# Performance work log

Hardware: AMD Instinct MI355X
Metric: run time of the kernel (lower is better)

## Reference

```python
import jax, jax.numpy as jnp
import numpy as np

B, E, S = 8, 128, 4096


def setup_inputs() -> dict:
    key = jax.random.key(0)
    ks = jax.random.split(key, 7)
    sc = 1.0 / np.sqrt(E)
    return {
        "x": jax.random.normal(ks[0], (B, E, S), dtype=jnp.float32),
        "Wq": jax.random.normal(ks[1], (E, E), dtype=jnp.float32) * sc,
        "bq": jax.random.normal(ks[2], (E,), dtype=jnp.float32) * 0.01,
        "Wk": jax.random.normal(ks[3], (E, E), dtype=jnp.float32) * sc,
        "bk": jax.random.normal(ks[4], (E,), dtype=jnp.float32) * 0.01,
        "Wv": jax.random.normal(ks[5], (E, E), dtype=jnp.float32) * sc,
        "bv": jax.random.normal(ks[6], (E,), dtype=jnp.float32) * 0.01,
    }


def reference(x, Wq, bq, Wk, bk, Wv, bv):
    # x: [B, E, S]; Conv1d(k=1) == per-position linear over channels.
    # Project then move to [B, S, E] (matches .permute(0, 2, 1)).
    Q = jnp.einsum('bes,fe->bsf', x, Wq) + bq  # [B, S, E]
    K = jnp.einsum('bes,fe->bsf', x, Wk) + bk
    V = jnp.einsum('bes,fe->bsf', x, Wv) + bv
    scale = jnp.sqrt(jnp.asarray(float(x.shape[1]), dtype=jnp.float32))
    attn = jnp.einsum('bqe,bke->bqk', Q, K) / scale  # [B, S, S]
    attn = jax.nn.softmax(attn, axis=2)
    out = jnp.einsum('bqk,bke->bqe', attn, V)  # [B, S, E]
    return out.transpose(0, 2, 1)  # [B, E, S]
```

## Files before the change

### kernel.cpp

```cpp
#include <hip/hip_runtime.h>
#include <math.h>

#define NB 8
#define NE 128
#define NS 4096
#define CSCALE 0.12751743f

typedef short s8v __attribute__((ext_vector_type(8)));
typedef float f4v __attribute__((ext_vector_type(4)));
typedef float f16v __attribute__((ext_vector_type(16)));
typedef unsigned int u32;
typedef unsigned int u2v __attribute__((ext_vector_type(2)));
typedef __attribute__((address_space(1))) const u32* gp1_t;
typedef __attribute__((address_space(3))) u32* lp3_t;

__device__ __forceinline__ ushort f2bf(float f) {
  union { float f; unsigned u; } v; v.f = f;
  unsigned r = v.u + 0x7fffu + ((v.u >> 16) & 1u);
  return (ushort)(r >> 16);
}
__device__ __forceinline__ float bf2f(ushort h) {
  union { unsigned u; float f; } v; v.u = ((unsigned)h) << 16; return v.f;
}
__device__ __forceinline__ void gload_lds16(const void* g, void* l) {
  __builtin_amdgcn_global_load_lds((gp1_t)g, (lp3_t)l, 16, 0, 0);
}
__device__ __forceinline__ u32 cvtpk(float lo, float hi) {
  u32 r;
  asm("v_cvt_pk_bf16_f32 %0, %1, %2" : "=v"(r) : "v"(lo), "v"(hi));
  return r;
}
__device__ __forceinline__ void split8(const float* __restrict__ p, float scale,
                                       s8v& hi, s8v& lo) {
  union { s8v v; ushort u[8]; } H, L;
  #pragma unroll
  for (int i = 0; i < 8; ++i) {
    float v = p[i] * scale;
    ushort h = f2bf(v);
    H.u[i] = h;
    L.u[i] = f2bf(v - bf2f(h));
  }
  hi = H.v; lo = L.v;
}

__global__ __launch_bounds__(256, 2) void proj_gemm(
    const float* __restrict__ x,
    const float* __restrict__ Wq, const float* __restrict__ bq,
    const float* __restrict__ Wk, const float* __restrict__ bk,
    const float* __restrict__ Wv, const float* __restrict__ bv,
    ushort* __restrict__ Qn, ushort* __restrict__ Kn, ushort* __restrict__ Vt)
{
  const int tid = threadIdx.x;
  const int wv = tid >> 6, lane = tid & 63;
  const int g = lane >> 4, c = lane & 15;
  const int bid = blockIdx.x;
  const int b = bid & 7;
  const int s0 = (bid >> 3) * 64;
  const float* xb = x + (size_t)b * NE * NS;

  __shared__ __align__(16) ushort xh[64][136], xl[64][136];

  {
    const int ss = tid & 63, cq = tid >> 6;
    #pragma unroll
    for (int p = 0; p < 4; ++p) {
      const int ch = p * 4 + cq;
      union { s8v v; ushort u[8]; } H, L;
      #pragma unroll
      for (int i = 0; i < 8; ++i) {
        float v = xb[(size_t)(ch * 8 + i) * NS + s0 + ss];
        ushort hi = f2bf(v);
        H.u[i] = hi;
        L.u[i] = f2bf(v - bf2f(hi));
      }
      *(s8v*)&xh[ss][ch * 8] = H.v;
      *(s8v*)&xl[ss][ch * 8] = L.v;
    }
  }
  __syncthreads();

  f4v aq[2][4], ak[2][4], av[2][4];
  #pragma unroll
  for (int i = 0; i < 2; ++i)
    #pragma unroll
    for (int j = 0; j < 4; ++j) {
      aq[i][j] = (f4v){0.f,0.f,0.f,0.f};
      ak[i][j] = (f4v){0.f,0.f,0.f,0.f};
      av[i][j] = (f4v){0.f,0.f,0.f,0.f};
    }

  #pragma unroll
  for (int ks = 0; ks < 4; ++ks) {
    s8v xbh[4], xbl[4];
    #pragma unroll
    for (int st = 0; st < 4; ++st) {
      xbh[st] = *(const s8v*)&xh[st * 16 + c][ks * 32 + g * 8];
      xbl[st] = *(const s8v*)&xl[st * 16 + c][ks * 32 + g * 8];
    }
    #pragma unroll
    for (int ftl = 0; ftl < 2; ++ftl) {
      const int f0 = (wv * 2 + ftl) * 16;
      const size_t wo = (size_t)(f0 + c) * NE + ks * 32 + g * 8;
      s8v qh, ql, kh, kl, vh, vl;
      split8(Wq + wo, CSCALE, qh, ql);
      split8(Wk + wo, 1.0f,   kh, kl);
      split8(Wv + wo, 1.0f,   vh, vl);
      #pragma unroll
      for (int st = 0; st < 4; ++st) {
        aq[ftl][st] = __builtin_amdgcn_mfma_f32_16x16x32_bf16(xbh[st], qh, aq[ftl][st], 0, 0, 0);
        aq[ftl][st] = __builtin_amdgcn_mfma_f32_16x16x32_bf16(xbl[st], qh, aq[ftl][st], 0, 0, 0);
        aq[ftl][st] = __builtin_amdgcn_mfma_f32_16x16x32_bf16(xbh[st], ql, aq[ftl][st], 0, 0, 0);
        av[ftl][st] = __builtin_amdgcn_mfma_f32_16x16x32_bf16(vh, xbh[st], av[ftl][st], 0, 0, 0);
        av[ftl][st] = __builtin_amdgcn_mfma_f32_16x16x32_bf16(vh, xbl[st], av[ftl][st], 0, 0, 0);
        av[ftl][st] = __builtin_amdgcn_mfma_f32_16x16x32_bf16(vl, xbh[st], av[ftl][st], 0, 0, 0);
        ak[ftl][st] = __builtin_amdgcn_mfma_f32_16x16x32_bf16(xbh[st], kh, ak[ftl][st], 0, 0, 0);
        ak[ftl][st] = __builtin_amdgcn_mfma_f32_16x16x32_bf16(xbl[st], kh, ak[ftl][st], 0, 0, 0);
        ak[ftl][st] = __builtin_amdgcn_mfma_f32_16x16x32_bf16(xbh[st], kl, ak[ftl][st], 0, 0, 0);
      }
    }
  }

  ushort* Qnb = Qn + (size_t)b * NS * NE;
  ushort* Knb = Kn + (size_t)b * NS * NE;
  ushort* Vtb = Vt + (size_t)b * NE * NS;
  #pragma unroll
  for (int ftl = 0; ftl < 2; ++ftl) {
    const int f0 = (wv * 2 + ftl) * 16;
    #pragma unroll
    for (int r = 0; r < 4; ++r) {
      const int f = f0 + 4 * g + r;
      const float bvv = bv[f];
      #pragma unroll
      for (int st = 0; st < 4; ++st)
        Vtb[(size_t)f * NS + s0 + st * 16 + c] = f2bf(av[ftl][st][r] + bvv);
    }
    const float bqv = bq[f0 + c] * CSCALE;
    const float bkv = bk[f0 + c];
    #pragma unroll
    for (int st = 0; st < 4; ++st)
      #pragma unroll
      for (int r = 0; r < 4; ++r) {
        const size_t ro = (size_t)(s0 + st * 16 + 4 * g + r) * NE + f0 + c;
        Qnb[ro] = f2bf(aq[ftl][st][r] + bqv);
        Knb[ro] = f2bf(ak[ftl][st][r] + bkv);
      }
  }
}

__global__ __launch_bounds__(256, 1) void attn_kernel(
    const ushort* __restrict__ Qn, const ushort* __restrict__ Kn,
    const ushort* __restrict__ Vt, float* __restrict__ out)
{
  const int tid = threadIdx.x;
  const int wv = tid >> 6, lane = tid & 63;
  const int h = lane >> 5, q5 = lane & 31;
  const int slice = wv >> 1;
  const int ws = wv & 1;
  const int bid = blockIdx.x;
  const int b = bid & 7;
  const int qw = (bid >> 3) * 128 + ws * 64;

  const ushort* Qb = Qn + (size_t)b * NS * NE;
  const char*   Kb = (const char*)(Kn + (size_t)b * NS * NE);
  const char*   Vb = (const char*)(Vt + (size_t)b * NE * NS);

  __shared__ __align__(16) char ldsK[2][2][16384];
  __shared__ __align__(16) char ldsV[2][2][16384];
  __shared__ float lx[2][2][32];

  s8v qf[2][8];
  #pragma unroll
  for (int u = 0; u < 2; ++u)
    #pragma unroll
    for (int dc = 0; dc < 8; ++dc)
      qf[u][dc] = *(const s8v*)(Qb + (size_t)(qw + u * 32 + q5) * NE + dc * 16 + h * 8);

  auto stage = [&](int buf, int t) {
    const int kt = slice * 32 + t;
    const char* Ksrc = Kb + (size_t)kt * (64 * 256);
    #pragma unroll
    for (int p = 0; p < 8; ++p) {
      const int off = ws * 8192 + p * 1024;
      const int lo = off + lane * 16;
      const int row = lo >> 8;
      gload_lds16(Ksrc + (lo ^ ((row & 15) << 4)), &ldsK[slice][buf][off]);
    }
    #pragma unroll
    for (int p = 0; p < 8; ++p) {
      const int off = ws * 8192 + p * 1024;
      const int lo = off + lane * 16;
      const int row = lo >> 7;
      const int inner = (lo & 127) ^ ((row & 7) << 4);
      gload_lds16(Vb + (size_t)row * (NS * 2) + kt * 128 + inner, &ldsV[slice][buf][off]);
    }
  };

  auto makefrag = [&](const float* p, int r0) -> s8v {
    u32 A = cvtpk(p[r0 + 0], p[r0 + 1]);
    u32 B = cvtpk(p[r0 + 4], p[r0 + 5]);
    u32 C = cvtpk(p[r0 + 2], p[r0 + 3]);
    u32 D = cvtpk(p[r0 + 6], p[r0 + 7]);
    u2v rAB = __builtin_amdgcn_permlane32_swap(A, B, false, false);
    u2v rCD = __builtin_amdgcn_permlane32_swap(C, D, false, false);
    union { s8v v; u32 w[4]; } P;
    P.w[0] = rAB[0]; P.w[1] = rCD[0]; P.w[2] = rAB[1]; P.w[3] = rCD[1];
    return P.v;
  };

  f16v oA[4], oB[4];
  #pragma unroll
  for (int dt = 0; dt < 4; ++dt) {
    oA[dt] = (f16v){0,0,0,0,0,0,0,0,0,0,0,0,0,0,0,0};
    oB[dt] = (f16v){0,0,0,0,0,0,0,0,0,0,0,0,0,0,0,0};
  }
  float lA = 0.f, lB = 0.f;

  stage(0, 0);
  asm volatile("s_waitcnt vmcnt(0)" ::: "memory");
  __syncthreads();

  #pragma unroll 1
  for (int t = 0; t < 32; ++t) {
    const int cur = t & 1;
    if (t + 1 < 32) stage(cur ^ 1, t + 1);
    const char* bK = ldsK[slice][cur];
    const char* bV = ldsV[slice][cur];

    #pragma unroll
    for (int kc = 0; kc < 2; ++kc) {
      f16v sA = (f16v){0,0,0,0,0,0,0,0,0,0,0,0,0,0,0,0};
      f16v sB = (f16v){0,0,0,0,0,0,0,0,0,0,0,0,0,0,0,0};
      #pragma unroll
      for (int dc = 0; dc < 8; ++dc) {
        s8v kf = *(const s8v*)(bK + (kc * 32 + q5) * 256 + ((dc * 32 + h * 16) ^ ((q5 & 15) << 4)));
        sA = __builtin_amdgcn_mfma_f32_32x32x16_bf16(kf, qf[0][dc], sA, 0, 0, 0);
        sB = __builtin_amdgcn_mfma_f32_32x32x16_bf16(kf, qf[1][dc], sB, 0, 0, 0);
      }
      float pA[16], pB[16];
      #pragma unroll
      for (int r = 0; r < 16; ++r) {
        pA[r] = __builtin_amdgcn_exp2f(sA[r]); lA += pA[r];
        pB[r] = __builtin_amdgcn_exp2f(sB[r]); lB += pB[r];
      }
      #pragma unroll
      for (int ksl = 0; ksl < 2; ++ksl) {
        s8v PA = makefrag(pA, ksl * 8);
        s8v PB = makefrag(pB, ksl * 8);
        const int ks = kc * 2 + ksl;
        #pragma unroll
        for (int dt = 0; dt < 4; ++dt) {
          s8v vf = *(const s8v*)(bV + (dt * 32 + q5) * 128 + ((ks * 32 + h * 16) ^ ((q5 & 7) << 4)));
          oA[dt] = __builtin_amdgcn_mfma_f32_32x32x16_bf16(vf, PA, oA[dt], 0, 0, 0);
          oB[dt] = __builtin_amdgcn_mfma_f32_32x32x16_bf16(vf, PB, oB[dt], 0, 0, 0);
        }
      }
    }
    asm volatile("s_waitcnt vmcnt(0)" ::: "memory");
    __syncthreads();
  }

  lA += __shfl_xor(lA, 32);
  lB += __shfl_xor(lB, 32);
  float* cb = (float*)&ldsK[0][0][0];
  if (slice == 1) {
    #pragma unroll
    for (int dt = 0; dt < 4; ++dt)
      #pragma unroll
      for (int r = 0; r < 16; ++r) {
        cb[ws * 8192 + (dt * 16 + r) * 64 + lane]      = oA[dt][r];
        cb[ws * 8192 + (64 + dt * 16 + r) * 64 + lane] = oB[dt][r];
      }
    if (h == 0) { lx[ws][0][q5] = lA; lx[ws][1][q5] = lB; }
  }
  __syncthreads();
  if (slice == 0) {
    const float rA = 1.0f / (lA + lx[ws][0][q5]);
    const float rB = 1.0f / (lB + lx[ws][1][q5]);
    float* ob = out + (size_t)b * NE * NS;
    #pragma unroll
    for (int dt = 0; dt < 4; ++dt)
      #pragma unroll
      for (int r = 0; r < 16; ++r) {
        const int e = dt * 32 + (r & 3) + 8 * (r >> 2) + 4 * h;
        ob[(size_t)e * NS + qw + q5] =
            (oA[dt][r] + cb[ws * 8192 + (dt * 16 + r) * 64 + lane]) * rA;
        ob[(size_t)e * NS + qw + 32 + q5] =
            (oB[dt][r] + cb[ws * 8192 + (64 + dt * 16 + r) * 64 + lane]) * rB;
      }
  }
}

extern "C" void kernel_launch(void* const* d_in, const int* in_sizes, int n_in,
                              void* d_out, int out_size, void* d_ws, size_t ws_size,
                              hipStream_t stream) {
  (void)in_sizes; (void)n_in; (void)out_size; (void)ws_size;
  const float* x  = (const float*)d_in[0];
  const float* Wq = (const float*)d_in[1];
  const float* bq = (const float*)d_in[2];
  const float* Wk = (const float*)d_in[3];
  const float* bk = (const float*)d_in[4];
  const float* Wv = (const float*)d_in[5];
  const float* bv = (const float*)d_in[6];
  float* out = (float*)d_out;

  ushort* Qn = (ushort*)d_ws;
  ushort* Kn = Qn + (size_t)NB * NS * NE;
  ushort* Vt = Kn + (size_t)NB * NS * NE;

  proj_gemm<<<dim3(NS / 64 * NB), 256, 0, stream>>>(x, Wq, bq, Wk, bk, Wv, bv, Qn, Kn, Vt);
  attn_kernel<<<dim3(NS / 128 * NB), 256, 0, stream>>>(Qn, Kn, Vt, out);
}
```

Baseline: 119.0 us.

## Split attention key range across four wave slices with 512-thread blocks

Each block now runs 8 waves instead of 4, so the key sequence is split into four slices of 32-key tiles instead of two slices of 64-key tiles. K and V staging is divided by wave group: one group loads K and the other loads V. The partial outputs and row sums from the four slices are combined through LDS in a serialized accumulation with a barrier per slice. The aim is more waves per CU to hide latency. The cost is a longer reduction epilogue and a tighter register budget from launch_bounds(512,2), which may cause spills given the large MFMA accumulators.

Result: slower. 131.5 us (+10.5%).

```diff
diff --git a/kernel.cpp b/kernel.cpp
--- a/kernel.cpp
+++ b/kernel.cpp
@@ -147,15 +147,15 @@
   }
 }
 
-__global__ __launch_bounds__(256, 1) void attn_kernel(
+__global__ __launch_bounds__(512, 2) void attn_kernel(
     const ushort* __restrict__ Qn, const ushort* __restrict__ Kn,
     const ushort* __restrict__ Vt, float* __restrict__ out)
 {
   const int tid = threadIdx.x;
   const int wv = tid >> 6, lane = tid & 63;
   const int h = lane >> 5, q5 = lane & 31;
-  const int slice = wv >> 1;
-  const int ws = wv & 1;
+  const int slice = wv & 3;
+  const int ws = wv >> 2;
   const int bid = blockIdx.x;
   const int b = bid & 7;
   const int qw = (bid >> 3) * 128 + ws * 64;
@@ -164,9 +164,11 @@
   const char*   Kb = (const char*)(Kn + (size_t)b * NS * NE);
   const char*   Vb = (const char*)(Vt + (size_t)b * NE * NS);
 
-  __shared__ __align__(16) char ldsK[2][2][16384];
-  __shared__ __align__(16) char ldsV[2][2][16384];
-  __shared__ float lx[2][2][32];
+  __shared__ __align__(16) char lds[131072];
+  __shared__ float lx[2][4][2][32];
+
+  auto Kbuf = [&](int sl, int bf) -> char* { return lds + (sl * 2 + bf) * 8192; };
+  auto Vbuf = [&](int sl, int bf) -> char* { return lds + 65536 + (sl * 2 + bf) * 8192; };
 
   s8v qf[2][8];
   #pragma unroll
@@ -177,21 +179,26 @@
 
   auto stage = [&](int buf, int t) {
     const int kt = slice * 32 + t;
-    const char* Ksrc = Kb + (size_t)kt * (64 * 256);
-    #pragma unroll
-    for (int p = 0; p < 8; ++p) {
-      const int off = ws * 8192 + p * 1024;
-      const int lo = off + lane * 16;
-      const int row = lo >> 8;
-      gload_lds16(Ksrc + (lo ^ ((row & 15) << 4)), &ldsK[slice][buf][off]);
-    }
-    #pragma unroll
-    for (int p = 0; p < 8; ++p) {
-      const int off = ws * 8192 + p * 1024;
-      const int lo = off + lane * 16;
-      const int row = lo >> 7;
-      const int inner = (lo & 127) ^ ((row & 7) << 4);
-      gload_lds16(Vb + (size_t)row * (NS * 2) + kt * 128 + inner, &ldsV[slice][buf][off]);
+    if (ws == 0) {
+      const char* Ksrc = Kb + (size_t)kt * (32 * 256);
+      char* dst = Kbuf(slice, buf);
+      #pragma unroll
+      for (int p = 0; p < 8; ++p) {
+        const int off = p * 1024;
+        const int lo = off + lane * 16;
+        const int row = lo >> 8;
+        gload_lds16(Ksrc + (lo ^ ((row & 15) << 4)), dst + off);
+      }
+    } else {
+      char* dst = Vbuf(slice, buf);
+      #pragma unroll
+      for (int p = 0; p < 8; ++p) {
+        const int off = p * 1024;
+        const int lo = off + lane * 16;
+        const int row = lo >> 6;
+        const int inner = (lo & 63) ^ ((row & 3) << 4);
+        gload_lds16(Vb + (size_t)row * (NS * 2) + kt * 64 + inner, dst + off);
+      }
     }
   };
 
@@ -223,36 +230,33 @@
   for (int t = 0; t < 32; ++t) {
     const int cur = t & 1;
     if (t + 1 < 32) stage(cur ^ 1, t + 1);
-    const char* bK = ldsK[slice][cur];
-    const char* bV = ldsV[slice][cur];
-
-    #pragma unroll
-    for (int kc = 0; kc < 2; ++kc) {
-      f16v sA = (f16v){0,0,0,0,0,0,0,0,0,0,0,0,0,0,0,0};
-      f16v sB = (f16v){0,0,0,0,0,0,0,0,0,0,0,0,0,0,0,0};
-      #pragma unroll
-      for (int dc = 0; dc < 8; ++dc) {
-        s8v kf = *(const s8v*)(bK + (kc * 32 + q5) * 256 + ((dc * 32 + h * 16) ^ ((q5 & 15) << 4)));
-        sA = __builtin_amdgcn_mfma_f32_32x32x16_bf16(kf, qf[0][dc], sA, 0, 0, 0);
-        sB = __builtin_amdgcn_mfma_f32_32x32x16_bf16(kf, qf[1][dc], sB, 0, 0, 0);
-      }
-      float pA[16], pB[16];
-      #pragma unroll
-      for (int r = 0; r < 16; ++r) {
-        pA[r] = __builtin_amdgcn_exp2f(sA[r]); lA += pA[r];
-        pB[r] = __builtin_amdgcn_exp2f(sB[r]); lB += pB[r];
-      }
-      #pragma unroll
-      for (int ksl = 0; ksl < 2; ++ksl) {
-        s8v PA = makefrag(pA, ksl * 8);
-        s8v PB = makefrag(pB, ksl * 8);
-        const int ks = kc * 2 + ksl;
-        #pragma unroll
-        for (int dt = 0; dt < 4; ++dt) {
-          s8v vf = *(const s8v*)(bV + (dt * 32 + q5) * 128 + ((ks * 32 + h * 16) ^ ((q5 & 7) << 4)));
-          oA[dt] = __builtin_amdgcn_mfma_f32_32x32x16_bf16(vf, PA, oA[dt], 0, 0, 0);
-          oB[dt] = __builtin_amdgcn_mfma_f32_32x32x16_bf16(vf, PB, oB[dt], 0, 0, 0);
-        }
+    const char* bK = Kbuf(slice, cur);
+    const char* bV = Vbuf(slice, cur);
+
+    f16v sA = (f16v){0,0,0,0,0,0,0,0,0,0,0,0,0,0,0,0};
+    f16v sB = (f16v){0,0,0,0,0,0,0,0,0,0,0,0,0,0,0,0};
+    #pragma unroll
+    for (int dc = 0; dc < 8; ++dc) {
+      s8v kf = *(const s8v*)(bK + q5 * 256 + ((dc * 32 + h * 16) ^ ((q5 & 15) << 4)));
+      sA = __builtin_amdgcn_mfma_f32_32x32x16_bf16(kf, qf[0][dc], sA, 0, 0, 0);
+      sB = __builtin_amdgcn_mfma_f32_32x32x16_bf16(kf, qf[1][dc], sB, 0, 0, 0);
+    }
+    float pA[16], pB[16];
+    #pragma unroll
+    for (int r = 0; r < 16; ++r) {
+      pA[r] = __builtin_amdgcn_exp2f(sA[r]); lA += pA[r];
+      pB[r] = __builtin_amdgcn_exp2f(sB[r]); lB += pB[r];
+    }
+    #pragma unroll
+    for (int ksl = 0; ksl < 2; ++ksl) {
+      s8v PA = makefrag(pA, ksl * 8);
+      s8v PB = makefrag(pB, ksl * 8);
+      #pragma unroll
+      for (int dt = 0; dt < 4; ++dt) {
+        const int vrow = dt * 32 + q5;
+        s8v vf = *(const s8v*)(bV + vrow * 64 + ((ksl * 32 + h * 16) ^ ((q5 & 3) << 4)));
+        oA[dt] = __builtin_amdgcn_mfma_f32_32x32x16_bf16(vf, PA, oA[dt], 0, 0, 0);
+        oB[dt] = __builtin_amdgcn_mfma_f32_32x32x16_bf16(vf, PB, oB[dt], 0, 0, 0);
       }
     }
     asm volatile("s_waitcnt vmcnt(0)" ::: "memory");
@@ -261,31 +265,47 @@
 
   lA += __shfl_xor(lA, 32);
   lB += __shfl_xor(lB, 32);
-  float* cb = (float*)&ldsK[0][0][0];
-  if (slice == 1) {
-    #pragma unroll
-    for (int dt = 0; dt < 4; ++dt)
-      #pragma unroll
-      for (int r = 0; r < 16; ++r) {
-        cb[ws * 8192 + (dt * 16 + r) * 64 + lane]      = oA[dt][r];
-        cb[ws * 8192 + (64 + dt * 16 + r) * 64 + lane] = oB[dt][r];
-      }
-    if (h == 0) { lx[ws][0][q5] = lA; lx[ws][1][q5] = lB; }
-  }
-  __syncthreads();
+  if (h == 0) { lx[ws][slice][0][q5] = lA; lx[ws][slice][1][q5] = lB; }
+  float* cb = (float*)lds;
+  const int base = ws * 8192;
   if (slice == 0) {
-    const float rA = 1.0f / (lA + lx[ws][0][q5]);
-    const float rB = 1.0f / (lB + lx[ws][1][q5]);
-    float* ob = out + (size_t)b * NE * NS;
     #pragma unroll
     for (int dt = 0; dt < 4; ++dt)
       #pragma unroll
       for (int r = 0; r < 16; ++r) {
         const int e = dt * 32 + (r & 3) + 8 * (r >> 2) + 4 * h;
-        ob[(size_t)e * NS + qw + q5] =
-            (oA[dt][r] + cb[ws * 8192 + (dt * 16 + r) * 64 + lane]) * rA;
-        ob[(size_t)e * NS + qw + 32 + q5] =
-            (oB[dt][r] + cb[ws * 8192 + (64 + dt * 16 + r) * 64 + lane]) * rB;
+        cb[base + e * 64 + q5]      = oA[dt][r];
+        cb[base + e * 64 + 32 + q5] = oB[dt][r];
+      }
+  }
+  __syncthreads();
+  #pragma unroll 1
+  for (int sl = 1; sl < 4; ++sl) {
+    if (slice == sl) {
+      #pragma unroll
+      for (int dt = 0; dt < 4; ++dt)
+        #pragma unroll
+        for (int r = 0; r < 16; ++r) {
+          const int e = dt * 32 + (r & 3) + 8 * (r >> 2) + 4 * h;
+          cb[base + e * 64 + q5]      += oA[dt][r];
+          cb[base + e * 64 + 32 + q5] += oB[dt][r];
+        }
+    }
+    __syncthreads();
+  }
+  if (slice == 0) {
+    const float rA = 1.0f / (lx[ws][0][0][q5] + lx[ws][1][0][q5] +
+                             lx[ws][2][0][q5] + lx[ws][3][0][q5]);
+    const float rB = 1.0f / (lx[ws][0][1][q5] + lx[ws][1][1][q5] +
+                             lx[ws][2][1][q5] + lx[ws][3][1][q5]);
+    float* ob = out + (size_t)b * NE * NS;
+    #pragma unroll
+    for (int dt = 0; dt < 4; ++dt)
+      #pragma unroll
+      for (int r = 0; r < 16; ++r) {
+        const int e = dt * 32 + (r & 3) + 8 * (r >> 2) + 4 * h;
+        ob[(size_t)e * NS + qw + q5]      = cb[base + e * 64 + q5] * rA;
+        ob[(size_t)e * NS + qw + 32 + q5] = cb[base + e * 64 + 32 + q5] * rB;
       }
   }
 }
@@ -308,5 +328,5 @@
   ushort* Vt = Kn + (size_t)NB * NS * NE;
 
   proj_gemm<<<dim3(NS / 64 * NB), 256, 0, stream>>>(x, Wq, bq, Wk, bk, Wv, bv, Qn, Kn, Vt);
-  attn_kernel<<<dim3(NS / 128 * NB), 256, 0, stream>>>(Qn, Kn, Vt, out);
-}
+  attn_kernel<<<dim3(NS / 128 * NB), 512, 0, stream>>>(Qn, Kn, Vt, out);
+}
```
